# Performance work log

Measured on AMD Instinct MI355X. Metric: run time of the kernel, lower is better.

The kernel has to match this reference:

```python
import jax, jax.numpy as jnp
import numpy as np

TEMPERATURE = 0.07
NEG = -9e15  # matches torch masked_fill value
EPS = 1e-8   # torch.nn.functional.cosine_similarity eps


def setup_inputs() -> dict:
    key = jax.random.key(0)
    k1, k2 = jax.random.split(key)
    B, D = 4096, 512
    return {
        "feats1": jax.random.normal(k1, (B, D), dtype=jnp.float32),
        "feats2": jax.random.normal(k2, (B, D), dtype=jnp.float32),
    }


def reference(feats1, feats2):
    feats = jnp.concatenate([feats1, feats2], axis=0)            # [2N, D]
    n = feats.shape[0]
    # cosine similarity via normalize-once + GEMM (same math as the
    # broadcasted F.cosine_similarity, incl. per-vector eps clamp)
    norms = jnp.maximum(jnp.linalg.norm(feats, axis=-1, keepdims=True), EPS)
    fn = feats / norms                                            # [2N, D]
    cos_sim = fn @ fn.T                                           # [2N, 2N]
    # mask self-similarity BEFORE temperature division (as in torch code)
    idx = jnp.arange(n)
    cos_sim = jnp.where(idx[:, None] == idx[None, :], NEG, cos_sim)
    cos_sim = cos_sim / TEMPERATURE
    # positive pair: eye rolled by N rows -> column (i + N) mod 2N
    pos_idx = (idx + n // 2) % n
    pos = cos_sim[idx, pos_idx]                                   # [2N]
    nll = jnp.mean(-pos + jax.nn.logsumexp(cos_sim, axis=-1))
    # ranking: rank of the positive among [pos, masked negatives];
    # equals # of masked entries strictly greater than pos
    masked = jnp.where(idx[None, :] == pos_idx[:, None], NEG, cos_sim)
    rank = jnp.sum(masked > pos[:, None], axis=-1)                # int [2N]
    acc_top1 = jnp.mean((rank == 0).astype(jnp.float32))
    acc_top5 = jnp.mean((rank < 5).astype(jnp.float32))
    acc_mean_pos = 1.0 + jnp.mean(rank.astype(jnp.float32))
    return (nll, acc_top1, acc_top5, acc_mean_pos)
```

## Files before the change

kernel.cpp:

```cpp
#include <hip/hip_runtime.h>
#include <math.h>
#include <stdint.h>

#define NTOT   8192
#define HALF_N 4096
#define DIM    512
#define INV_T  14.2857142857142857f
#define NTILE  64
#define NBLK   2080

using s16x8 = __attribute__((ext_vector_type(8))) short;
using f32x4 = __attribute__((ext_vector_type(4))) float;

__device__ unsigned short g_fnb[NTOT * DIM];
__device__ float g_pos[NTOT];
__device__ float g_ps[(size_t)NTILE * NTOT];
__device__ int   g_pc[(size_t)NTILE * NTOT];
__device__ float g_part4[32 * 4];
__device__ int   g_tick2;

__constant__ int c_pre[11] = {0,136,392,648,904,1040,1296,1552,1688,1944,2080};
__constant__ int c_gi[10]  = {0,0,0,0,1,1,1,2,2,3};
__constant__ int c_gj[10]  = {0,1,2,3,1,2,3,2,3,3};

__device__ __forceinline__ float bf2f(unsigned short u) {
  union { unsigned int i; float f; } v; v.i = ((unsigned int)u) << 16; return v.f;
}
__device__ __forceinline__ unsigned short f2bf(float x) {
  union { float f; unsigned int i; } v; v.f = x;
  unsigned int u = v.i;
  return (unsigned short)((u + 0x7FFFu + ((u >> 16) & 1u)) >> 16);
}

__device__ __forceinline__ void gload16(const unsigned short* g, unsigned short* l) {
  __builtin_amdgcn_global_load_lds(
      (const __attribute__((address_space(1))) unsigned int*)g,
      (__attribute__((address_space(3))) unsigned int*)l, 16, 0, 0);
}

__global__ __launch_bounds__(256) void knorm(const float* __restrict__ f1,
                                             const float* __restrict__ f2) {
  const int tid  = threadIdx.x;
  const int wv   = tid >> 6;
  const int pi   = wv >> 1;
  const int half = wv & 1;
  const int lane = tid & 63;
  const int b    = blockIdx.x * 2 + pi;
  const int row  = b + half * HALF_N;

  if (blockIdx.x == 0 && tid == 0)
    __hip_atomic_store(&g_tick2, 0, __ATOMIC_RELAXED, __HIP_MEMORY_SCOPE_AGENT);

  const float* src = (half == 0) ? (f1 + (size_t)b * DIM) : (f2 + (size_t)b * DIM);
  float4 v0 = ((const float4*)src)[lane];
  float4 v1 = ((const float4*)src)[lane + 64];
  float ss = v0.x*v0.x + v0.y*v0.y + v0.z*v0.z + v0.w*v0.w
           + v1.x*v1.x + v1.y*v1.y + v1.z*v1.z + v1.w*v1.w;
  #pragma unroll
  for (int o = 32; o >= 1; o >>= 1) ss += __shfl_xor(ss, o, 64);
  const float sc = 1.0f / fmaxf(sqrtf(ss), 1e-8f);
  ushort4 h0, h1;
  h0.x = f2bf(v0.x * sc); h0.y = f2bf(v0.y * sc);
  h0.z = f2bf(v0.z * sc); h0.w = f2bf(v0.w * sc);
  h1.x = f2bf(v1.x * sc); h1.y = f2bf(v1.y * sc);
  h1.z = f2bf(v1.z * sc); h1.w = f2bf(v1.w * sc);
  ushort4* dst = (ushort4*)(g_fnb + (size_t)row * DIM);
  dst[lane]      = h0;
  dst[lane + 64] = h1;

  __shared__ ushort4 sh[2][64][2];
  if (half == 1) { sh[pi][lane][0] = h0; sh[pi][lane][1] = h1; }
  __syncthreads();
  if (half == 0) {
    const ushort4 p0 = sh[pi][lane][0], p1 = sh[pi][lane][1];
    float s = bf2f(h0.x)*bf2f(p0.x) + bf2f(h0.y)*bf2f(p0.y)
            + bf2f(h0.z)*bf2f(p0.z) + bf2f(h0.w)*bf2f(p0.w)
            + bf2f(h1.x)*bf2f(p1.x) + bf2f(h1.y)*bf2f(p1.y)
            + bf2f(h1.z)*bf2f(p1.z) + bf2f(h1.w)*bf2f(p1.w);
    #pragma unroll
    for (int o = 32; o >= 1; o >>= 1) s += __shfl_xor(s, o, 64);
    if (lane == 0) { g_pos[b] = s; g_pos[b + HALF_N] = s; }
  }
}

__global__ __launch_bounds__(256, 4) void kmain() {
  __shared__ __align__(16) unsigned short As[128 * 64];
  __shared__ __align__(16) unsigned short Bs[128 * 64];
  float* sRowS = reinterpret_cast<float*>(As);
  int*   sRowC = reinterpret_cast<int*>(sRowS + 128);
  float* sColS = reinterpret_cast<float*>(sRowC + 128);
  int*   sColC = reinterpret_cast<int*>(sColS + 128);

  const int t_sw = (blockIdx.x & 7) * (NBLK / 8) + (blockIdx.x >> 3);
  int sp = 0;
  while (t_sw >= c_pre[sp + 1]) ++sp;
  int l = t_sw - c_pre[sp];
  int lbi, lbj;
  if (c_gi[sp] == c_gj[sp]) {
    int r16 = 16; lbi = 0;
    while (l >= r16) { l -= r16; --r16; ++lbi; }
    lbj = lbi + l;
  } else {
    lbi = l >> 4; lbj = l & 15;
  }
  const int bi = c_gi[sp] * 16 + lbi;
  const int bj = c_gj[sp] * 16 + lbj;
  const bool offdiag = (bi != bj);
  const int i0 = bi * 128, j0 = bj * 128;

  const int tid  = threadIdx.x;
  const int lane = tid & 63;
  const int w    = tid >> 6;
  const int wr   = (w >> 1) * 64;
  const int wc   = (w & 1) * 64;
  const int lrow = lane & 15;
  const int lq   = lane >> 4;

  const int rsub = lane >> 3;
  const int lcb  = (lane & 7) ^ rsub;
  const unsigned short* Ag = g_fnb + (size_t)(i0 + w * 32 + rsub) * DIM + lcb * 8;
  const unsigned short* Bg = g_fnb + (size_t)(j0 + w * 32 + rsub) * DIM + lcb * 8;
  unsigned short* Al = &As[w * 32 * 64];
  unsigned short* Bl = &Bs[w * 32 * 64];

  f32x4 acc[4][4];
  #pragma unroll
  for (int a = 0; a < 4; ++a)
    #pragma unroll
    for (int bb = 0; bb < 4; ++bb) { acc[a][bb][0]=0.f; acc[a][bb][1]=0.f; acc[a][bb][2]=0.f; acc[a][bb][3]=0.f; }

  const unsigned short* Bls = offdiag ? (const unsigned short*)Bs
                                      : (const unsigned short*)As;

  for (int kt = 0; kt < 8; ++kt) {
    __syncthreads();
    const int kb = kt * 64;
    #pragma unroll
    for (int q = 0; q < 4; ++q) {
      gload16(Ag + (size_t)(q * 8) * DIM + kb, Al + q * 512);
      if (offdiag) gload16(Bg + (size_t)(q * 8) * DIM + kb, Bl + q * 512);
    }
    __syncthreads();

    #pragma unroll
    for (int kk = 0; kk < 2; ++kk) {
      s16x8 af[4], bf[4];
      #pragma unroll
      for (int mi = 0; mi < 4; ++mi) {
        const int r = wr + mi * 16 + lrow;
        af[mi] = *(const s16x8*)(&As[r * 64 + (((kk * 4 + lq) ^ (lrow & 7)) * 8)]);
      }
      #pragma unroll
      for (int ni = 0; ni < 4; ++ni) {
        const int r = wc + ni * 16 + lrow;
        bf[ni] = *(const s16x8*)(&Bls[r * 64 + (((kk * 4 + lq) ^ (lrow & 7)) * 8)]);
      }
      #pragma unroll
      for (int mi = 0; mi < 4; ++mi)
        #pragma unroll
        for (int ni = 0; ni < 4; ++ni)
          acc[mi][ni] = __builtin_amdgcn_mfma_f32_16x16x32_bf16(af[mi], bf[ni], acc[mi][ni], 0, 0, 0);
    }
  }

  __syncthreads();
  if (tid < 128) { sRowS[tid] = 0.f; sRowC[tid] = 0; sColS[tid] = 0.f; sColC[tid] = 0; }
  __syncthreads();

  #pragma unroll
  for (int mi = 0; mi < 4; ++mi) {
    #pragma unroll
    for (int r = 0; r < 4; ++r) {
      const int ridx = wr + mi * 16 + lq * 4 + r;
      const int i  = i0 + ridx;
      const float pv = g_pos[i];
      float s = 0.f; int c = 0;
      #pragma unroll
      for (int ni = 0; ni < 4; ++ni) {
        const int j = j0 + wc + ni * 16 + lrow;
        const float v = acc[mi][ni][r];
        const float e = __expf(v * INV_T);
        const bool diag = (j == i);
        s += diag ? 0.f : e;
        c += (!diag && (j != (i ^ HALF_N)) && (v > pv)) ? 1 : 0;
      }
      #pragma unroll
      for (int o = 1; o < 16; o <<= 1) {
        s += __shfl_xor(s, o, 64);
        c += __shfl_xor(c, o, 64);
      }
      if (lrow == 0) {
        atomicAdd(&sRowS[ridx], s);
        atomicAdd(&sRowC[ridx], c);
      }
    }
  }

  if (offdiag) {
    #pragma unroll
    for (int ni = 0; ni < 4; ++ni) {
      const int cidx = wc + ni * 16 + lrow;
      const int j  = j0 + cidx;
      const float pj = g_pos[j];
      float s = 0.f; int c = 0;
      #pragma unroll
      for (int mi = 0; mi < 4; ++mi) {
        #pragma unroll
        for (int r = 0; r < 4; ++r) {
          const int i = i0 + wr + mi * 16 + lq * 4 + r;
          const float v = acc[mi][ni][r];
          s += __expf(v * INV_T);
          c += ((i != (j ^ HALF_N)) && (v > pj)) ? 1 : 0;
        }
      }
      s += __shfl_xor(s, 16, 64); s += __shfl_xor(s, 32, 64);
      c += __shfl_xor(c, 16, 64); c += __shfl_xor(c, 32, 64);
      if (lq == 0) {
        atomicAdd(&sColS[cidx], s);
        atomicAdd(&sColC[cidx], c);
      }
    }
  }
  __syncthreads();

  if (tid < 128) {
    g_ps[(size_t)bj * NTOT + i0 + tid] = sRowS[tid];
    g_pc[(size_t)bj * NTOT + i0 + tid] = sRowC[tid];
  } else if (offdiag && tid < 256) {
    const int r2 = tid - 128;
    g_ps[(size_t)bi * NTOT + j0 + r2] = sColS[r2];
    g_pc[(size_t)bi * NTOT + j0 + r2] = sColC[r2];
  }
}

__global__ __launch_bounds__(256) void kredfin(float* __restrict__ out) {
  const int tid = threadIdx.x;
  const int i = blockIdx.x * 256 + tid;
  float s = 0.f; int c = 0;
  #pragma unroll 8
  for (int sl = 0; sl < NTILE; ++sl) {
    s += g_ps[(size_t)sl * NTOT + i];
    c += g_pc[(size_t)sl * NTOT + i];
  }
  float nll = -g_pos[i] * INV_T + logf(s);
  float t1 = (c == 0) ? 1.f : 0.f;
  float t5 = (c < 5) ? 1.f : 0.f;
  float mr = (float)c;
  #pragma unroll
  for (int o = 32; o >= 1; o >>= 1) {
    nll += __shfl_xor(nll, o, 64);
    t1  += __shfl_xor(t1, o, 64);
    t5  += __shfl_xor(t5, o, 64);
    mr  += __shfl_xor(mr, o, 64);
  }
  __shared__ float red[4][4];
  const int wv = tid >> 6, lane = tid & 63;
  if (lane == 0) { red[wv][0] = nll; red[wv][1] = t1; red[wv][2] = t5; red[wv][3] = mr; }
  __syncthreads();
  if (tid == 0) {
    float a = 0.f, b = 0.f, cc = 0.f, d = 0.f;
    #pragma unroll
    for (int k = 0; k < 4; ++k) { a += red[k][0]; b += red[k][1]; cc += red[k][2]; d += red[k][3]; }
    g_part4[blockIdx.x * 4 + 0] = a;
    g_part4[blockIdx.x * 4 + 1] = b;
    g_part4[blockIdx.x * 4 + 2] = cc;
    g_part4[blockIdx.x * 4 + 3] = d;
    __builtin_amdgcn_fence(__ATOMIC_RELEASE, "agent");
    const int old = __hip_atomic_fetch_add(&g_tick2, 1,
                        __ATOMIC_RELAXED, __HIP_MEMORY_SCOPE_AGENT);
    if (old == 31) {
      __builtin_amdgcn_fence(__ATOMIC_ACQUIRE, "agent");
      float A = 0.f, B = 0.f, C = 0.f, D = 0.f;
      for (int k = 0; k < 32; ++k) {
        A += g_part4[k * 4 + 0];
        B += g_part4[k * 4 + 1];
        C += g_part4[k * 4 + 2];
        D += g_part4[k * 4 + 3];
      }
      out[0] = A / (float)NTOT;
      out[1] = B / (float)NTOT;
      out[2] = C / (float)NTOT;
      out[3] = 1.f + D / (float)NTOT;
    }
  }
}

extern "C" void kernel_launch(void* const* d_in, const int* in_sizes, int n_in,
                              void* d_out, int out_size, void* d_ws, size_t ws_size,
                              hipStream_t stream) {
  const float* f1 = (const float*)d_in[0];
  const float* f2 = (const float*)d_in[1];
  float* out = (float*)d_out;

  knorm  <<<dim3(2048), dim3(256), 0, stream>>>(f1, f2);
  kmain  <<<dim3(NBLK), dim3(256), 0, stream>>>();
  kredfin<<<dim3(32),   dim3(256), 0, stream>>>(out);
}
```

Measured before the change: 147.3 us.

## Pair two column tiles per block to reuse A tile in symmetric GEMM

Each block now processes one 128-row A tile against two adjacent 128-column B tiles, sharing the A tile loads and A fragment reads across both. Block count drops by about half, and the triangular schedule is remapped with a per-row prefix table. A second accumulator set and B buffer are added, so register and LDS use grow and the launch-bounds occupancy hint is lowered from 4 to 2 blocks per CU. Epilogues run sequentially with extra barriers.

Result: slower. 157.8 us (+7.2%).

```diff
diff --git a/kernel.cpp b/kernel.cpp
--- a/kernel.cpp
+++ b/kernel.cpp
@@ -7,7 +7,7 @@
 #define DIM    512
 #define INV_T  14.2857142857142857f
 #define NTILE  64
-#define NBLK   2080
+#define NBLK   1056
 
 using s16x8 = __attribute__((ext_vector_type(8))) short;
 using f32x4 = __attribute__((ext_vector_type(4))) float;
@@ -19,9 +19,12 @@
 __device__ float g_part4[32 * 4];
 __device__ int   g_tick2;
 
-__constant__ int c_pre[11] = {0,136,392,648,904,1040,1296,1552,1688,1944,2080};
-__constant__ int c_gi[10]  = {0,0,0,0,1,1,1,2,2,3};
-__constant__ int c_gj[10]  = {0,1,2,3,1,2,3,2,3,3};
+__constant__ int c_rpre[65] = {
+  0,32,64,95,126,156,186,215,244,272,300,327,354,380,406,431,456,
+  480,504,527,550,572,594,615,636,656,676,695,714,732,750,767,784,
+  800,816,831,846,860,874,887,900,912,924,935,946,956,966,975,984,
+  992,1000,1007,1014,1020,1026,1031,1036,1040,1044,1047,1050,1052,
+  1054,1055,1056};
 
 __device__ __forceinline__ float bf2f(unsigned short u) {
   union { unsigned int i; float f; } v; v.i = ((unsigned int)u) << 16; return v.f;
@@ -83,30 +86,28 @@
   }
 }
 
-__global__ __launch_bounds__(256, 4) void kmain() {
-  __shared__ __align__(16) unsigned short As[128 * 64];
-  __shared__ __align__(16) unsigned short Bs[128 * 64];
+__global__ __launch_bounds__(256, 2) void kmain() {
+  __shared__ __align__(16) unsigned short As [128 * 64];
+  __shared__ __align__(16) unsigned short Bs0[128 * 64];
+  __shared__ __align__(16) unsigned short Bs1[128 * 64];
   float* sRowS = reinterpret_cast<float*>(As);
   int*   sRowC = reinterpret_cast<int*>(sRowS + 128);
   float* sColS = reinterpret_cast<float*>(sRowC + 128);
   int*   sColC = reinterpret_cast<int*>(sColS + 128);
 
   const int t_sw = (blockIdx.x & 7) * (NBLK / 8) + (blockIdx.x >> 3);
-  int sp = 0;
-  while (t_sw >= c_pre[sp + 1]) ++sp;
-  int l = t_sw - c_pre[sp];
-  int lbi, lbj;
-  if (c_gi[sp] == c_gj[sp]) {
-    int r16 = 16; lbi = 0;
-    while (l >= r16) { l -= r16; --r16; ++lbi; }
-    lbj = lbi + l;
+  int bi = 0;
+  while (t_sw >= c_rpre[bi + 1]) ++bi;
+  const int p = t_sw - c_rpre[bi];
+  int bj0, bj1, nsub;
+  if (bi & 1) {
+    if (p == 0) { bj0 = bi; bj1 = bi; nsub = 1; }
+    else        { bj0 = bi + 2 * p - 1; bj1 = bj0 + 1; nsub = 2; }
   } else {
-    lbi = l >> 4; lbj = l & 15;
-  }
-  const int bi = c_gi[sp] * 16 + lbi;
-  const int bj = c_gj[sp] * 16 + lbj;
-  const bool offdiag = (bi != bj);
-  const int i0 = bi * 128, j0 = bj * 128;
+    bj0 = bi + 2 * p; bj1 = bj0 + 1; nsub = 2;
+  }
+  const bool off0 = (bj0 != bi);
+  const int i0 = bi * 128;
 
   const int tid  = threadIdx.x;
   const int lane = tid & 63;
@@ -118,19 +119,24 @@
 
   const int rsub = lane >> 3;
   const int lcb  = (lane & 7) ^ rsub;
-  const unsigned short* Ag = g_fnb + (size_t)(i0 + w * 32 + rsub) * DIM + lcb * 8;
-  const unsigned short* Bg = g_fnb + (size_t)(j0 + w * 32 + rsub) * DIM + lcb * 8;
-  unsigned short* Al = &As[w * 32 * 64];
-  unsigned short* Bl = &Bs[w * 32 * 64];
-
-  f32x4 acc[4][4];
+  const unsigned short* Ag  = g_fnb + (size_t)(i0 + w * 32 + rsub) * DIM + lcb * 8;
+  const unsigned short* B0g = g_fnb + (size_t)(bj0 * 128 + w * 32 + rsub) * DIM + lcb * 8;
+  const unsigned short* B1g = g_fnb + (size_t)(bj1 * 128 + w * 32 + rsub) * DIM + lcb * 8;
+  unsigned short* Al  = &As [w * 32 * 64];
+  unsigned short* B0l = &Bs0[w * 32 * 64];
+  unsigned short* B1l = &Bs1[w * 32 * 64];
+
+  f32x4 acc0[4][4], acc1[4][4];
   #pragma unroll
   for (int a = 0; a < 4; ++a)
     #pragma unroll
-    for (int bb = 0; bb < 4; ++bb) { acc[a][bb][0]=0.f; acc[a][bb][1]=0.f; acc[a][bb][2]=0.f; acc[a][bb][3]=0.f; }
-
-  const unsigned short* Bls = offdiag ? (const unsigned short*)Bs
-                                      : (const unsigned short*)As;
+    for (int bb = 0; bb < 4; ++bb) {
+      acc0[a][bb][0]=0.f; acc0[a][bb][1]=0.f; acc0[a][bb][2]=0.f; acc0[a][bb][3]=0.f;
+      acc1[a][bb][0]=0.f; acc1[a][bb][1]=0.f; acc1[a][bb][2]=0.f; acc1[a][bb][3]=0.f;
+    }
+
+  const unsigned short* B0ls = off0 ? (const unsigned short*)Bs0
+                                    : (const unsigned short*)As;
 
   for (int kt = 0; kt < 8; ++kt) {
     __syncthreads();
@@ -138,7 +144,8 @@
     #pragma unroll
     for (int q = 0; q < 4; ++q) {
       gload16(Ag + (size_t)(q * 8) * DIM + kb, Al + q * 512);
-      if (offdiag) gload16(Bg + (size_t)(q * 8) * DIM + kb, Bl + q * 512);
+      if (off0)      gload16(B0g + (size_t)(q * 8) * DIM + kb, B0l + q * 512);
+      if (nsub == 2) gload16(B1g + (size_t)(q * 8) * DIM + kb, B1l + q * 512);
     }
     __syncthreads();
 
@@ -153,84 +160,104 @@
       #pragma unroll
       for (int ni = 0; ni < 4; ++ni) {
         const int r = wc + ni * 16 + lrow;
-        bf[ni] = *(const s16x8*)(&Bls[r * 64 + (((kk * 4 + lq) ^ (lrow & 7)) * 8)]);
+        bf[ni] = *(const s16x8*)(&B0ls[r * 64 + (((kk * 4 + lq) ^ (lrow & 7)) * 8)]);
       }
       #pragma unroll
       for (int mi = 0; mi < 4; ++mi)
         #pragma unroll
         for (int ni = 0; ni < 4; ++ni)
-          acc[mi][ni] = __builtin_amdgcn_mfma_f32_16x16x32_bf16(af[mi], bf[ni], acc[mi][ni], 0, 0, 0);
-    }
-  }
-
+          acc0[mi][ni] = __builtin_amdgcn_mfma_f32_16x16x32_bf16(af[mi], bf[ni], acc0[mi][ni], 0, 0, 0);
+      if (nsub == 2) {
+        s16x8 bg[4];
+        #pragma unroll
+        for (int ni = 0; ni < 4; ++ni) {
+          const int r = wc + ni * 16 + lrow;
+          bg[ni] = *(const s16x8*)(&Bs1[r * 64 + (((kk * 4 + lq) ^ (lrow & 7)) * 8)]);
+        }
+        #pragma unroll
+        for (int mi = 0; mi < 4; ++mi)
+          #pragma unroll
+          for (int ni = 0; ni < 4; ++ni)
+            acc1[mi][ni] = __builtin_amdgcn_mfma_f32_16x16x32_bf16(af[mi], bg[ni], acc1[mi][ni], 0, 0, 0);
+      }
+    }
+  }
   __syncthreads();
-  if (tid < 128) { sRowS[tid] = 0.f; sRowC[tid] = 0; sColS[tid] = 0.f; sColC[tid] = 0; }
-  __syncthreads();
-
-  #pragma unroll
-  for (int mi = 0; mi < 4; ++mi) {
-    #pragma unroll
-    for (int r = 0; r < 4; ++r) {
-      const int ridx = wr + mi * 16 + lq * 4 + r;
-      const int i  = i0 + ridx;
-      const float pv = g_pos[i];
-      float s = 0.f; int c = 0;
+
+  auto epi = [&](f32x4 (&acc)[4][4], int bj, bool offd) {
+    const int j0 = bj * 128;
+    if (tid < 128) { sRowS[tid] = 0.f; sRowC[tid] = 0; sColS[tid] = 0.f; sColC[tid] = 0; }
+    __syncthreads();
+
+    #pragma unroll
+    for (int mi = 0; mi < 4; ++mi) {
+      #pragma unroll
+      for (int r = 0; r < 4; ++r) {
+        const int ridx = wr + mi * 16 + lq * 4 + r;
+        const int i  = i0 + ridx;
+        const float pv = g_pos[i];
+        float s = 0.f; int c = 0;
+        #pragma unroll
+        for (int ni = 0; ni < 4; ++ni) {
+          const int j = j0 + wc + ni * 16 + lrow;
+          const float v = acc[mi][ni][r];
+          const float e = __expf(v * INV_T);
+          const bool diag = (j == i);
+          s += diag ? 0.f : e;
+          c += (!diag && (j != (i ^ HALF_N)) && (v > pv)) ? 1 : 0;
+        }
+        #pragma unroll
+        for (int o = 1; o < 16; o <<= 1) {
+          s += __shfl_xor(s, o, 64);
+          c += __shfl_xor(c, o, 64);
+        }
+        if (lrow == 0) {
+          atomicAdd(&sRowS[ridx], s);
+          atomicAdd(&sRowC[ridx], c);
+        }
+      }
+    }
+
+    if (offd) {
       #pragma unroll
       for (int ni = 0; ni < 4; ++ni) {
-        const int j = j0 + wc + ni * 16 + lrow;
-        const float v = acc[mi][ni][r];
-        const float e = __expf(v * INV_T);
-        const bool diag = (j == i);
-        s += diag ? 0.f : e;
-        c += (!diag && (j != (i ^ HALF_N)) && (v > pv)) ? 1 : 0;
-      }
-      #pragma unroll
-      for (int o = 1; o < 16; o <<= 1) {
-        s += __shfl_xor(s, o, 64);
-        c += __shfl_xor(c, o, 64);
-      }
-      if (lrow == 0) {
-        atomicAdd(&sRowS[ridx], s);
-        atomicAdd(&sRowC[ridx], c);
-      }
-    }
-  }
-
-  if (offdiag) {
-    #pragma unroll
-    for (int ni = 0; ni < 4; ++ni) {
-      const int cidx = wc + ni * 16 + lrow;
-      const int j  = j0 + cidx;
-      const float pj = g_pos[j];
-      float s = 0.f; int c = 0;
-      #pragma unroll
-      for (int mi = 0; mi < 4; ++mi) {
-        #pragma unroll
-        for (int r = 0; r < 4; ++r) {
-          const int i = i0 + wr + mi * 16 + lq * 4 + r;
-          const float v = acc[mi][ni][r];
-          s += __expf(v * INV_T);
-          c += ((i != (j ^ HALF_N)) && (v > pj)) ? 1 : 0;
-        }
-      }
-      s += __shfl_xor(s, 16, 64); s += __shfl_xor(s, 32, 64);
-      c += __shfl_xor(c, 16, 64); c += __shfl_xor(c, 32, 64);
-      if (lq == 0) {
-        atomicAdd(&sColS[cidx], s);
-        atomicAdd(&sColC[cidx], c);
-      }
-    }
-  }
-  __syncthreads();
-
-  if (tid < 128) {
-    g_ps[(size_t)bj * NTOT + i0 + tid] = sRowS[tid];
-    g_pc[(size_t)bj * NTOT + i0 + tid] = sRowC[tid];
-  } else if (offdiag && tid < 256) {
-    const int r2 = tid - 128;
-    g_ps[(size_t)bi * NTOT + j0 + r2] = sColS[r2];
-    g_pc[(size_t)bi * NTOT + j0 + r2] = sColC[r2];
-  }
+        const int cidx = wc + ni * 16 + lrow;
+        const int j  = j0 + cidx;
+        const float pj = g_pos[j];
+        float s = 0.f; int c = 0;
+        #pragma unroll
+        for (int mi = 0; mi < 4; ++mi) {
+          #pragma unroll
+          for (int r = 0; r < 4; ++r) {
+            const int i = i0 + wr + mi * 16 + lq * 4 + r;
+            const float v = acc[mi][ni][r];
+            s += __expf(v * INV_T);
+            c += ((i != (j ^ HALF_N)) && (v > pj)) ? 1 : 0;
+          }
+        }
+        s += __shfl_xor(s, 16, 64); s += __shfl_xor(s, 32, 64);
+        c += __shfl_xor(c, 16, 64); c += __shfl_xor(c, 32, 64);
+        if (lq == 0) {
+          atomicAdd(&sColS[cidx], s);
+          atomicAdd(&sColC[cidx], c);
+        }
+      }
+    }
+    __syncthreads();
+
+    if (tid < 128) {
+      g_ps[(size_t)bj * NTOT + i0 + tid] = sRowS[tid];
+      g_pc[(size_t)bj * NTOT + i0 + tid] = sRowC[tid];
+    } else if (offd && tid < 256) {
+      const int r2 = tid - 128;
+      g_ps[(size_t)bi * NTOT + j0 + r2] = sColS[r2];
+      g_pc[(size_t)bi * NTOT + j0 + r2] = sColC[r2];
+    }
+    __syncthreads();
+  };
+
+  epi(acc0, bj0, off0);
+  if (nsub == 2) epi(acc1, bj1, true);
 }
 
 __global__ __launch_bounds__(256) void kredfin(float* __restrict__ out) {
```
